# Kernel tuning notes

Hardware: AMD Instinct MI355X
Metric: run time of the kernel (lower is better)

Reference implementation:

```python
import jax, jax.numpy as jnp
import numpy as np

EMBED_DIM = 768
NUM_HEADS = 12


def setup_inputs() -> dict:
    key = jax.random.key(0)
    ks = jax.random.split(key, 9)
    C = EMBED_DIM
    x = jax.random.normal(ks[0], (8, 3136, C), dtype=jnp.float32)
    s = 0.02
    Wq = jax.random.normal(ks[1], (C, C), dtype=jnp.float32) * s
    Wk = jax.random.normal(ks[2], (C, C), dtype=jnp.float32) * s
    Wv = jax.random.normal(ks[3], (C, C), dtype=jnp.float32) * s
    Wo = jax.random.normal(ks[4], (C, C), dtype=jnp.float32) * s
    bq = jax.random.normal(ks[5], (C,), dtype=jnp.float32) * s
    bk = jax.random.normal(ks[6], (C,), dtype=jnp.float32) * s
    bv = jax.random.normal(ks[7], (C,), dtype=jnp.float32) * s
    bo = jax.random.normal(ks[8], (C,), dtype=jnp.float32) * s
    return {"x": x, "Wq": Wq, "bq": bq, "Wk": Wk, "bk": bk,
            "Wv": Wv, "bv": bv, "Wo": Wo, "bo": bo, "T": 16}


def reference(x, Wq, bq, Wk, bk, Wv, bv, Wo, bo, T):
    B, N, C = x.shape
    H = NUM_HEADS
    hd = C // H
    Hh = H // 2
    P = N // T
    scale = 1.0 / np.sqrt(hd).astype(np.float32)

    Q = (x @ Wq + bq).reshape(B, T, P, H, hd)
    K = (x @ Wk + bk).reshape(B, T, P, H, hd)
    V = (x @ Wv + bv).reshape(B, T, P, H, hd)

    # spatial attention: first Hh heads, attend over patches within each frame
    Qs, Ks, Vs = Q[..., :Hh, :], K[..., :Hh, :], V[..., :Hh, :]
    scores_s = jnp.einsum('btphd,btqhd->bthpq', Qs, Ks) * scale  # (B,T,Hh,P,P)
    ws = jax.nn.softmax(scores_s, axis=-1)
    out_s = jnp.einsum('bthpq,btqhd->btphd', ws, Vs)  # (B,T,P,Hh,hd)

    # temporal attention: last Hh heads, attend over frames at each patch
    Qt, Kt, Vt = Q[..., Hh:, :], K[..., Hh:, :], V[..., Hh:, :]
    scores_t = jnp.einsum('btphd,bsphd->bphts', Qt, Kt) * scale  # (B,P,Hh,T,T)
    wt = jax.nn.softmax(scores_t, axis=-1)
    out_t = jnp.einsum('bphts,bsphd->btphd', wt, Vt)  # (B,T,P,Hh,hd)

    out = jnp.concatenate([out_s, out_t], axis=3).reshape(B, N, C)
    return out @ Wo + bo
```

## Files before the change

kernel.cpp:

```cpp
#include <hip/hip_runtime.h>


typedef __attribute__((ext_vector_type(8))) short short8;
typedef __attribute__((ext_vector_type(4))) float f32x4;

typedef __attribute__((address_space(1))) void gvoid;
typedef __attribute__((address_space(3))) void lvoid;

__device__ __forceinline__ unsigned short f2b(float f) {
  unsigned int u = __float_as_uint(f);
  unsigned int r = (u + 0x7FFFu + ((u >> 16) & 1u)) >> 16;
  return (unsigned short)r;
}

__global__ __launch_bounds__(256) void k_convert_x(
    const float* __restrict__ x, unsigned short* __restrict__ xb,
    const float* __restrict__ bq, const float* __restrict__ bk,
    const float* __restrict__ bv, float* __restrict__ bqkv) {
  int tid = blockIdx.x * 256 + threadIdx.x;
  if (tid < 2304)
    bqkv[tid] = tid < 768 ? bq[tid] : (tid < 1536 ? bk[tid - 768] : bv[tid - 1536]);
  float4 v = ((const float4*)x)[tid];
  ushort4 o;
  o.x = f2b(v.x); o.y = f2b(v.y); o.z = f2b(v.z); o.w = f2b(v.w);
  ((ushort4*)xb)[tid] = o;
}

__global__ __launch_bounds__(256) void k_pack_w(
    const float* __restrict__ Wq, const float* __restrict__ Wk,
    const float* __restrict__ Wv, const float* __restrict__ Wo,
    unsigned short* __restrict__ wqkvT, unsigned short* __restrict__ woT) {
  __shared__ float tile[32][33];
  int bid = blockIdx.x;
  const float* W;
  unsigned short* dst;
  int n0, k0;
  if (bid < 1728) {
    int tn = bid % 72, tk = bid / 72;
    n0 = tn * 32; k0 = tk * 32;
    int which = n0 / 768;
    W = which == 0 ? Wq : (which == 1 ? Wk : Wv);
    dst = wqkvT;
  } else {
    int b2 = bid - 1728;
    int tn = b2 % 24, tk = b2 / 24;
    n0 = tn * 32; k0 = tk * 32;
    W = Wo; dst = woT;
  }
  int nn0 = n0 % 768;
  for (int i = threadIdx.x; i < 1024; i += 256) {
    int r = i >> 5, c = i & 31;
    tile[r][c] = W[(size_t)(k0 + r) * 768 + nn0 + c];
  }
  __syncthreads();
  for (int i = threadIdx.x; i < 1024; i += 256) {
    int r = i >> 5, c = i & 31;
    dst[(size_t)(n0 + r) * 768 + k0 + c] = f2b(tile[c][r]);
  }
}


#define FENCE asm volatile("" ::: "memory")
#define BARRIER do { FENCE; __builtin_amdgcn_s_barrier(); FENCE; } while (0)
#define WAIT_LGKM0 asm volatile("s_waitcnt lgkmcnt(0)" ::: "memory")
#define WAIT_VM6 asm volatile("s_waitcnt vmcnt(6)" ::: "memory")

#define STAGE(PBASE, BUFBASE, HT, KT_) do {                                          \
    int kt__ = (KT_);                                                                \
    bool real__ = (kt__ < 12);                                                       \
    if (!real__) kt__ -= 12;                                                         \
    const unsigned short* src__ = (PBASE) + (HT) * 98304 + kt__ * 64;                \
    unsigned d0__ = real__ ? ((BUFBASE) + (HT) * 8192 + w * 512) : (65536u + w * 512); \
    unsigned d1__ = real__ ? ((BUFBASE) + (HT) * 8192 + 4096 + w * 512) : (65536u + w * 512); \
    __builtin_amdgcn_global_load_lds((const gvoid*)src__, (lvoid*)(lds + d0__), 16, 0, 0); \
    __builtin_amdgcn_global_load_lds((const gvoid*)(src__ + 49152), (lvoid*)(lds + d1__), 16, 0, 0); \
  } while (0)

#define LDA(MH, ABASE) do {                                                          \
    const unsigned short* ab__ = lds + (ABASE) + ((MH) * 128 + arow) * 64;           \
    _Pragma("unroll")                                                                \
    for (int mf = 0; mf < 4; ++mf) {                                                 \
      af[mf][0] = *(const short8*)(ab__ + mf * 1024 + s0);                           \
      af[mf][1] = *(const short8*)(ab__ + mf * 1024 + s1);                           \
    }                                                                                \
  } while (0)

#define LDB(NH, BBASE) do {                                                          \
    const unsigned short* bb__ = lds + (BBASE) + ((NH) * 128 + brow) * 64;           \
    _Pragma("unroll")                                                                \
    for (int nf = 0; nf < 2; ++nf) {                                                 \
      bf[nf][0] = *(const short8*)(bb__ + nf * 1024 + s0);                           \
      bf[nf][1] = *(const short8*)(bb__ + nf * 1024 + s1);                           \
    }                                                                                \
  } while (0)

#define MM(MH, NH) do {                                                              \
    __builtin_amdgcn_s_setprio(1);                                                   \
    _Pragma("unroll")                                                                \
    for (int mf = 0; mf < 4; ++mf) {                                                 \
      _Pragma("unroll")                                                              \
      for (int nf = 0; nf < 2; ++nf) {                                               \
        acc[MH][mf][NH][nf] = __builtin_amdgcn_mfma_f32_16x16x32_bf16(               \
            af[mf][0], bf[nf][0], acc[MH][mf][NH][nf], 0, 0, 0);                     \
        acc[MH][mf][NH][nf] = __builtin_amdgcn_mfma_f32_16x16x32_bf16(               \
            af[mf][1], bf[nf][1], acc[MH][mf][NH][nf], 0, 0, 0);                     \
      }                                                                              \
    }                                                                                \
    __builtin_amdgcn_s_setprio(0);                                                   \
  } while (0)

__global__ __launch_bounds__(512, 2) void k_gemm256(
    const unsigned short* __restrict__ A, const unsigned short* __restrict__ Bt,
    const float* __restrict__ bias, unsigned short* __restrict__ Cout,
    int M, int N) {
  __shared__ __align__(16) unsigned short lds[69632];
  const int nwg = gridDim.x;
  const int nbx = N >> 8;
  const int orig = blockIdx.x;
  const int q = nwg >> 3, r = nwg & 7;
  const int xcd = orig & 7, lin = orig >> 3;
  const int wg = (xcd < r ? xcd * (q + 1) : r * (q + 1) + (xcd - r) * q) + lin;
  const int m0 = (wg / nbx) << 8, n0 = (wg % nbx) << 8;

  const int tid = threadIdx.x;
  const int w = tid >> 6, l = tid & 63;
  const int wm = w >> 2, wn = w & 3;
  const int lg = l >> 4, ln = l & 15;
  const int arow = wm * 64 + ln;
  const int brow = wn * 32 + ln;
  const int s0 = (lg ^ (ln & 7)) * 8;
  const int s1 = s0 ^ 32;
  const int srow = tid >> 3;
  const int slg8 = ((tid & 7) ^ (srow & 7)) * 8;
  const unsigned short* pA = A + (size_t)(m0 + srow) * 768 + slg8;
  const unsigned short* pB = Bt + (size_t)(n0 + srow) * 768 + slg8;

  f32x4 acc[2][4][2][2] = {};

  STAGE(pA, 0,     0, 0);
  STAGE(pB, 16384, 1, 0);
  STAGE(pA, 0,     1, 0);
  STAGE(pB, 16384, 0, 0);
  STAGE(pA, 32768, 0, 1);
  STAGE(pB, 49152, 1, 1);
  STAGE(pA, 32768, 1, 1);
  asm volatile("s_waitcnt vmcnt(6)" ::: "memory");
  __builtin_amdgcn_s_barrier();
  FENCE;

  for (int it = 0; it < 6; ++it) {
    const int kt1 = 2 * it + 1, ktn0 = 2 * it + 2, ktn1 = 2 * it + 3;
    short8 af[4][2], bf[2][2];
    LDA(0, 0); LDB(0, 16384);
    STAGE(pB, 49152, 0, kt1);
    BARRIER; WAIT_LGKM0; MM(0, 0); BARRIER;
    LDB(1, 16384);
    STAGE(pA, 0, 0, ktn0);
    BARRIER; WAIT_LGKM0; MM(0, 1); BARRIER;
    LDA(1, 0);
    STAGE(pB, 16384, 1, ktn0);
    BARRIER; WAIT_LGKM0; MM(1, 1); BARRIER;
    LDB(0, 16384);
    STAGE(pA, 0, 1, ktn0);
    WAIT_VM6;
    BARRIER; WAIT_LGKM0; MM(1, 0); BARRIER;
    LDA(0, 32768); LDB(0, 49152);
    STAGE(pB, 16384, 0, ktn0);
    BARRIER; WAIT_LGKM0; MM(0, 0); BARRIER;
    LDB(1, 49152);
    STAGE(pA, 32768, 0, ktn1);
    BARRIER; WAIT_LGKM0; MM(0, 1); BARRIER;
    LDA(1, 32768);
    STAGE(pB, 49152, 1, ktn1);
    BARRIER; WAIT_LGKM0; MM(1, 1); BARRIER;
    LDB(0, 49152);
    STAGE(pA, 32768, 1, ktn1);
    WAIT_VM6;
    BARRIER; WAIT_LGKM0; MM(1, 0); BARRIER;
  }

#pragma unroll
  for (int mh = 0; mh < 2; ++mh)
#pragma unroll
    for (int mf = 0; mf < 4; ++mf)
#pragma unroll
      for (int nh = 0; nh < 2; ++nh)
#pragma unroll
        for (int nf = 0; nf < 2; ++nf) {
          const int col = n0 + nh * 128 + wn * 32 + nf * 16 + ln;
          const float bval = bias[col];
          const int row = m0 + mh * 128 + wm * 64 + mf * 16 + lg * 4;
#pragma unroll
          for (int rr = 0; rr < 4; ++rr)
            Cout[(size_t)(row + rr) * N + col] = f2b(acc[mh][mf][nh][nf][rr] + bval);
        }
}

__global__ __launch_bounds__(256) void k_gemm_out(
    const unsigned short* __restrict__ A, const unsigned short* __restrict__ Bt,
    const float* __restrict__ bias, float* __restrict__ C,
    int M, int N, int K) {
  __shared__ __align__(16) unsigned short As[2][128 * 32];
  __shared__ __align__(16) unsigned short Bs[2][128 * 32];
  const int tid = threadIdx.x;
  const int w = tid >> 6, l = tid & 63;
  const int lg = l >> 4, ln = l & 15;
  const int m0 = blockIdx.y * 128, n0 = blockIdx.x * 128;
  const int wr = (w >> 1) * 64, wc = (w & 1) * 64;
  f32x4 acc[4][4] = {};
  const unsigned short* ga = A + (size_t)(m0 + (tid >> 2)) * K + ((tid & 3) * 8);
  const unsigned short* gb = Bt + (size_t)(n0 + (tid >> 2)) * K + ((tid & 3) * 8);
  const size_t krow64 = (size_t)64 * K;
  const int wofs = w * 512;

#define OSTAGE(CO, K0) do {                                                                        \
    __builtin_amdgcn_global_load_lds((const gvoid*)(ga + (K0)),          (lvoid*)(&As[0][0] + (CO) + wofs),        16, 0, 0); \
    __builtin_amdgcn_global_load_lds((const gvoid*)(ga + krow64 + (K0)), (lvoid*)(&As[0][0] + (CO) + 2048 + wofs), 16, 0, 0); \
    __builtin_amdgcn_global_load_lds((const gvoid*)(gb + (K0)),          (lvoid*)(&Bs[0][0] + (CO) + wofs),        16, 0, 0); \
    __builtin_amdgcn_global_load_lds((const gvoid*)(gb + krow64 + (K0)), (lvoid*)(&Bs[0][0] + (CO) + 2048 + wofs), 16, 0, 0); \
  } while (0)

  OSTAGE(0, 0);
  asm volatile("s_waitcnt vmcnt(0)" ::: "memory");
  BARRIER;
  int co = 0;
  for (int k0 = 0; k0 < K; k0 += 32) {
    if (k0 + 32 < K) OSTAGE(co ^ 4096, k0 + 32);
    const unsigned short* as = &As[0][0] + co;
    const unsigned short* bs = &Bs[0][0] + co;
    short8 a[4], b[4];
#pragma unroll
    for (int mt = 0; mt < 4; ++mt)
      a[mt] = *(const short8*)(as + (wr + mt * 16 + ln) * 32 + lg * 8);
#pragma unroll
    for (int nt = 0; nt < 4; ++nt)
      b[nt] = *(const short8*)(bs + (wc + nt * 16 + ln) * 32 + lg * 8);
#pragma unroll
    for (int mt = 0; mt < 4; ++mt)
#pragma unroll
      for (int nt = 0; nt < 4; ++nt)
        acc[mt][nt] = __builtin_amdgcn_mfma_f32_16x16x32_bf16(a[mt], b[nt], acc[mt][nt], 0, 0, 0);
    asm volatile("s_waitcnt vmcnt(0)" ::: "memory");
    BARRIER;
    co ^= 4096;
  }
#pragma unroll
  for (int nt = 0; nt < 4; ++nt) {
    int col = n0 + wc + nt * 16 + ln;
    float bval = bias[col];
#pragma unroll
    for (int mt = 0; mt < 4; ++mt) {
      int row = m0 + wr + mt * 16 + lg * 4;
#pragma unroll
      for (int r = 0; r < 4; ++r)
        C[(size_t)(row + r) * N + col] = acc[mt][nt][r] + bval;
    }
  }
#undef OSTAGE
}

__global__ __launch_bounds__(256) void k_attn_spatial(
    const unsigned short* __restrict__ qkv, unsigned short* __restrict__ attn) {
  const int bi = blockIdx.x;
  const int h = bi % 6;
  const int t = (bi / 6) % 16;
  const int b = bi / 96;
  const int base_row = b * 3136 + t * 196;
  __shared__ __align__(16) unsigned short Vt[64][232];
  __shared__ __align__(16) unsigned short Pl[4][16][232];
  for (int i = threadIdx.x; i < 196 * 64; i += 256) {
    int key = i >> 6, d = i & 63;
    Vt[d][key] = qkv[(size_t)(base_row + key) * 2304 + 1536 + h * 64 + d];
  }
  for (int i = threadIdx.x; i < 64 * 28; i += 256)
    Vt[i / 28][196 + (i % 28)] = 0;
  __syncthreads();
  const int w = threadIdx.x >> 6, l = threadIdx.x & 63;
  const int lg = l >> 4, ln = l & 15;
  const float scale = 0.125f;
  for (int mt = w; mt < 13; mt += 4) {
    int qm = mt * 16 + ln; if (qm > 195) qm = 195;
    const size_t qoff = (size_t)(base_row + qm) * 2304 + h * 64 + lg * 8;
    short8 qa0 = *(const short8*)(qkv + qoff);
    short8 qa1 = *(const short8*)(qkv + qoff + 32);
    f32x4 st[13];
#pragma unroll
    for (int nt = 0; nt < 13; ++nt) {
      int kn = nt * 16 + ln; if (kn > 195) kn = 195;
      const size_t koff = (size_t)(base_row + kn) * 2304 + 768 + h * 64 + lg * 8;
      short8 kb0 = *(const short8*)(qkv + koff);
      short8 kb1 = *(const short8*)(qkv + koff + 32);
      f32x4 s = {0.f, 0.f, 0.f, 0.f};
      s = __builtin_amdgcn_mfma_f32_16x16x32_bf16(qa0, kb0, s, 0, 0, 0);
      s = __builtin_amdgcn_mfma_f32_16x16x32_bf16(qa1, kb1, s, 0, 0, 0);
      st[nt] = s;
    }
    float mr[4] = {-1e30f, -1e30f, -1e30f, -1e30f};
#pragma unroll
    for (int nt = 0; nt < 13; ++nt) {
      bool valid = (nt * 16 + ln) < 196;
#pragma unroll
      for (int r = 0; r < 4; ++r) {
        float v = valid ? st[nt][r] * scale : -1e30f;
        st[nt][r] = v;
        mr[r] = fmaxf(mr[r], v);
      }
    }
#pragma unroll
    for (int msk = 1; msk <= 8; msk <<= 1)
#pragma unroll
      for (int r = 0; r < 4; ++r) mr[r] = fmaxf(mr[r], __shfl_xor(mr[r], msk));
    float sm[4] = {0.f, 0.f, 0.f, 0.f};
#pragma unroll
    for (int nt = 0; nt < 13; ++nt)
#pragma unroll
      for (int r = 0; r < 4; ++r) {
        float p = __expf(st[nt][r] - mr[r]);
        st[nt][r] = p;
        sm[r] += p;
      }
#pragma unroll
    for (int msk = 1; msk <= 8; msk <<= 1)
#pragma unroll
      for (int r = 0; r < 4; ++r) sm[r] += __shfl_xor(sm[r], msk);
    float inv[4];
#pragma unroll
    for (int r = 0; r < 4; ++r) inv[r] = 1.f / sm[r];
#pragma unroll
    for (int nt = 0; nt < 13; ++nt)
#pragma unroll
      for (int r = 0; r < 4; ++r)
        Pl[w][lg * 4 + r][nt * 16 + ln] = f2b(st[nt][r] * inv[r]);
#pragma unroll
    for (int r = 0; r < 4; ++r) Pl[w][ln][208 + lg * 4 + r] = 0;
#pragma unroll
    for (int nt4 = 0; nt4 < 4; ++nt4) {
      f32x4 acc = {0.f, 0.f, 0.f, 0.f};
#pragma unroll
      for (int ks = 0; ks < 7; ++ks) {
        short8 pa = *(const short8*)(&Pl[w][ln][ks * 32 + lg * 8]);
        short8 vb = *(const short8*)(&Vt[nt4 * 16 + ln][ks * 32 + lg * 8]);
        acc = __builtin_amdgcn_mfma_f32_16x16x32_bf16(pa, vb, acc, 0, 0, 0);
      }
#pragma unroll
      for (int r = 0; r < 4; ++r) {
        int m = mt * 16 + lg * 4 + r;
        if (m < 196)
          attn[(size_t)(base_row + m) * 768 + h * 64 + nt4 * 16 + ln] = f2b(acc[r]);
      }
    }
  }
}

__global__ __launch_bounds__(256) void k_attn_temporal(
    const unsigned short* __restrict__ qkv, unsigned short* __restrict__ attn) {
  const int w = threadIdx.x >> 6, l = threadIdx.x & 63;
  const int u = blockIdx.x * 4 + w;
  const int b = u / 1176;
  const int rem = u % 1176;
  const int p = rem / 6;
  const int h = 6 + rem % 6;
  const size_t rowb = (size_t)b * 3136 + p;
  __shared__ __align__(16) unsigned short Vt[4][64][40];
  __shared__ __align__(16) unsigned short Pl[4][16][40];
  for (int i = l; i < 1024; i += 64) {
    int tt = i >> 6, d = i & 63;
    Vt[w][d][tt] = qkv[(rowb + (size_t)tt * 196) * 2304 + 1536 + h * 64 + d];
  }
  for (int i = l; i < 1024; i += 64)
    Vt[w][i >> 4][16 + (i & 15)] = 0;
  const int lg = l >> 4, ln = l & 15;
  const size_t qoff = (rowb + (size_t)ln * 196) * 2304 + h * 64 + lg * 8;
  short8 qa0 = *(const short8*)(qkv + qoff);
  short8 qa1 = *(const short8*)(qkv + qoff + 32);
  short8 kb0 = *(const short8*)(qkv + qoff + 768);
  short8 kb1 = *(const short8*)(qkv + qoff + 768 + 32);
  f32x4 s = {0.f, 0.f, 0.f, 0.f};
  s = __builtin_amdgcn_mfma_f32_16x16x32_bf16(qa0, kb0, s, 0, 0, 0);
  s = __builtin_amdgcn_mfma_f32_16x16x32_bf16(qa1, kb1, s, 0, 0, 0);
  const float scale = 0.125f;
  float stv[4], mr[4];
#pragma unroll
  for (int r = 0; r < 4; ++r) { stv[r] = s[r] * scale; mr[r] = stv[r]; }
#pragma unroll
  for (int msk = 1; msk <= 8; msk <<= 1)
#pragma unroll
    for (int r = 0; r < 4; ++r) mr[r] = fmaxf(mr[r], __shfl_xor(mr[r], msk));
  float sm[4];
#pragma unroll
  for (int r = 0; r < 4; ++r) { stv[r] = __expf(stv[r] - mr[r]); sm[r] = stv[r]; }
#pragma unroll
  for (int msk = 1; msk <= 8; msk <<= 1)
#pragma unroll
    for (int r = 0; r < 4; ++r) sm[r] += __shfl_xor(sm[r], msk);
#pragma unroll
  for (int r = 0; r < 4; ++r)
    Pl[w][lg * 4 + r][ln] = f2b(stv[r] / sm[r]);
#pragma unroll
  for (int r = 0; r < 4; ++r) Pl[w][ln][16 + lg * 4 + r] = 0;
  short8 pa = *(const short8*)(&Pl[w][ln][lg * 8]);
#pragma unroll
  for (int nt4 = 0; nt4 < 4; ++nt4) {
    short8 vb = *(const short8*)(&Vt[w][nt4 * 16 + ln][lg * 8]);
    f32x4 acc = {0.f, 0.f, 0.f, 0.f};
    acc = __builtin_amdgcn_mfma_f32_16x16x32_bf16(pa, vb, acc, 0, 0, 0);
#pragma unroll
    for (int r = 0; r < 4; ++r) {
      int tq = lg * 4 + r;
      attn[((size_t)b * 3136 + (size_t)tq * 196 + p) * 768 + h * 64 + nt4 * 16 + ln] = f2b(acc[r]);
    }
  }
}

extern "C" void kernel_launch(void* const* d_in, const int* in_sizes, int n_in,
                              void* d_out, int out_size, void* d_ws, size_t ws_size,
                              hipStream_t stream) {
  const float* x  = (const float*)d_in[0];
  const float* Wq = (const float*)d_in[1];
  const float* bq = (const float*)d_in[2];
  const float* Wk = (const float*)d_in[3];
  const float* bk = (const float*)d_in[4];
  const float* Wv = (const float*)d_in[5];
  const float* bv = (const float*)d_in[6];
  const float* Wo = (const float*)d_in[7];
  const float* bo = (const float*)d_in[8];
  float* out = (float*)d_out;
  char* ws = (char*)d_ws;
  unsigned short* xb    = (unsigned short*)(ws + 0);
  unsigned short* wqkvT = (unsigned short*)(ws + 38535168);
  float*          bqkv  = (float*)(ws + 42074112);
  unsigned short* woT   = (unsigned short*)(ws + 42083328);
  unsigned short* qkvb  = (unsigned short*)(ws + 43262976);
  unsigned short* attnb = (unsigned short*)(ws + 158868480);

  k_convert_x<<<18816, 256, 0, stream>>>(x, xb, bq, bk, bv, bqkv);
  k_pack_w<<<2304, 256, 0, stream>>>(Wq, Wk, Wv, Wo, wqkvT, woT);
  k_gemm256<<<882, 512, 0, stream>>>(xb, wqkvT, bqkv, qkvb, 25088, 2304);
  k_attn_spatial<<<768, 256, 0, stream>>>(qkvb, attnb);
  k_attn_temporal<<<2352, 256, 0, stream>>>(qkvb, attnb);
  k_gemm_out<<<dim3(6, 196), 256, 0, stream>>>(attnb, woT, bo, out, 25088, 768, 768);
}
```

Before: 255.2 us.

## Merge spatial and temporal attention into one launch and rework GEMM pipeline

Spatial and temporal attention now run as one kernel that dispatches on block index, so the two launches become one and the work can overlap. Spatial blocks are split in half by query tiles, which doubles the block count for better occupancy but loads V twice. Separately, the QKV GEMM's staging order is rotated, the trailing barrier after each MFMA step is removed, and the wait threshold drops from vmcnt 6 to 4. These changes aim to cut synchronisation stalls, at the risk of LDS hazards if the rotated staging overwrites a buffer that is still being read.

```diff
diff --git a/kernel.cpp b/kernel.cpp
--- a/kernel.cpp
+++ b/kernel.cpp
@@ -63,7 +63,7 @@
 #define FENCE asm volatile("" ::: "memory")
 #define BARRIER do { FENCE; __builtin_amdgcn_s_barrier(); FENCE; } while (0)
 #define WAIT_LGKM0 asm volatile("s_waitcnt lgkmcnt(0)" ::: "memory")
-#define WAIT_VM6 asm volatile("s_waitcnt vmcnt(6)" ::: "memory")
+#define WAIT_VM4 asm volatile("s_waitcnt vmcnt(4)" ::: "memory")
 
 #define STAGE(PBASE, BUFBASE, HT, KT_) do {                                          \
     int kt__ = (KT_);                                                                \
@@ -138,45 +138,43 @@
   f32x4 acc[2][4][2][2] = {};
 
   STAGE(pA, 0,     0, 0);
+  STAGE(pB, 16384, 0, 0);
+  STAGE(pA, 0,     1, 0);
   STAGE(pB, 16384, 1, 0);
-  STAGE(pA, 0,     1, 0);
-  STAGE(pB, 16384, 0, 0);
   STAGE(pA, 32768, 0, 1);
   STAGE(pB, 49152, 1, 1);
-  STAGE(pA, 32768, 1, 1);
-  asm volatile("s_waitcnt vmcnt(6)" ::: "memory");
-  __builtin_amdgcn_s_barrier();
-  FENCE;
+  WAIT_VM4;
+  BARRIER;
 
   for (int it = 0; it < 6; ++it) {
     const int kt1 = 2 * it + 1, ktn0 = 2 * it + 2, ktn1 = 2 * it + 3;
     short8 af[4][2], bf[2][2];
     LDA(0, 0); LDB(0, 16384);
+    STAGE(pA, 32768, 1, kt1);
+    BARRIER; WAIT_LGKM0; MM(0, 0);
+    LDB(1, 16384);
     STAGE(pB, 49152, 0, kt1);
-    BARRIER; WAIT_LGKM0; MM(0, 0); BARRIER;
-    LDB(1, 16384);
+    BARRIER; WAIT_LGKM0; MM(0, 1);
+    LDA(1, 0);
     STAGE(pA, 0, 0, ktn0);
-    BARRIER; WAIT_LGKM0; MM(0, 1); BARRIER;
-    LDA(1, 0);
+    BARRIER; WAIT_LGKM0; MM(1, 1);
+    LDB(0, 16384);
     STAGE(pB, 16384, 1, ktn0);
-    BARRIER; WAIT_LGKM0; MM(1, 1); BARRIER;
-    LDB(0, 16384);
+    WAIT_VM4;
+    BARRIER; WAIT_LGKM0; MM(1, 0);
+    LDA(0, 32768); LDB(0, 49152);
     STAGE(pA, 0, 1, ktn0);
-    WAIT_VM6;
-    BARRIER; WAIT_LGKM0; MM(1, 0); BARRIER;
-    LDA(0, 32768); LDB(0, 49152);
+    BARRIER; WAIT_LGKM0; MM(0, 0);
+    LDB(1, 49152);
     STAGE(pB, 16384, 0, ktn0);
-    BARRIER; WAIT_LGKM0; MM(0, 0); BARRIER;
-    LDB(1, 49152);
+    BARRIER; WAIT_LGKM0; MM(0, 1);
+    LDA(1, 32768);
     STAGE(pA, 32768, 0, ktn1);
-    BARRIER; WAIT_LGKM0; MM(0, 1); BARRIER;
-    LDA(1, 32768);
+    BARRIER; WAIT_LGKM0; MM(1, 1);
+    LDB(0, 49152);
     STAGE(pB, 49152, 1, ktn1);
-    BARRIER; WAIT_LGKM0; MM(1, 1); BARRIER;
-    LDB(0, 49152);
-    STAGE(pA, 32768, 1, ktn1);
-    WAIT_VM6;
-    BARRIER; WAIT_LGKM0; MM(1, 0); BARRIER;
+    WAIT_VM4;
+    BARRIER; WAIT_LGKM0; MM(1, 0);
   }
 
 #pragma unroll
@@ -259,155 +257,155 @@
 #undef OSTAGE
 }
 
-__global__ __launch_bounds__(256) void k_attn_spatial(
+__global__ __launch_bounds__(256) void k_attn_fused(
     const unsigned short* __restrict__ qkv, unsigned short* __restrict__ attn) {
-  const int bi = blockIdx.x;
-  const int h = bi % 6;
-  const int t = (bi / 6) % 16;
-  const int b = bi / 96;
-  const int base_row = b * 3136 + t * 196;
-  __shared__ __align__(16) unsigned short Vt[64][232];
-  __shared__ __align__(16) unsigned short Pl[4][16][232];
-  for (int i = threadIdx.x; i < 196 * 64; i += 256) {
-    int key = i >> 6, d = i & 63;
-    Vt[d][key] = qkv[(size_t)(base_row + key) * 2304 + 1536 + h * 64 + d];
-  }
-  for (int i = threadIdx.x; i < 64 * 28; i += 256)
-    Vt[i / 28][196 + (i % 28)] = 0;
-  __syncthreads();
+  __shared__ __align__(16) unsigned short smem[29696];
   const int w = threadIdx.x >> 6, l = threadIdx.x & 63;
   const int lg = l >> 4, ln = l & 15;
   const float scale = 0.125f;
-  for (int mt = w; mt < 13; mt += 4) {
-    int qm = mt * 16 + ln; if (qm > 195) qm = 195;
-    const size_t qoff = (size_t)(base_row + qm) * 2304 + h * 64 + lg * 8;
+  if (blockIdx.x < 1536) {
+    const int bi = blockIdx.x >> 1;
+    const int half = blockIdx.x & 1;
+    const int h = bi % 6;
+    const int t = (bi / 6) % 16;
+    const int b = bi / 96;
+    const int base_row = b * 3136 + t * 196;
+    unsigned short* Vt = smem;
+    unsigned short* Pl = smem + 14848;
+    for (int i = threadIdx.x; i < 196 * 64; i += 256) {
+      int key = i >> 6, d = i & 63;
+      Vt[d * 232 + key] = qkv[(size_t)(base_row + key) * 2304 + 1536 + h * 64 + d];
+    }
+    for (int i = threadIdx.x; i < 64 * 28; i += 256)
+      Vt[(i / 28) * 232 + 196 + (i % 28)] = 0;
+    __syncthreads();
+    const int r0 = half ? 7 : 0, r1 = half ? 13 : 7;
+    for (int mt = r0 + w; mt < r1; mt += 4) {
+      int qm = mt * 16 + ln; if (qm > 195) qm = 195;
+      const size_t qoff = (size_t)(base_row + qm) * 2304 + h * 64 + lg * 8;
+      short8 qa0 = *(const short8*)(qkv + qoff);
+      short8 qa1 = *(const short8*)(qkv + qoff + 32);
+      f32x4 st[13];
+#pragma unroll
+      for (int nt = 0; nt < 13; ++nt) {
+        int kn = nt * 16 + ln; if (kn > 195) kn = 195;
+        const size_t koff = (size_t)(base_row + kn) * 2304 + 768 + h * 64 + lg * 8;
+        short8 kb0 = *(const short8*)(qkv + koff);
+        short8 kb1 = *(const short8*)(qkv + koff + 32);
+        f32x4 s = {0.f, 0.f, 0.f, 0.f};
+        s = __builtin_amdgcn_mfma_f32_16x16x32_bf16(qa0, kb0, s, 0, 0, 0);
+        s = __builtin_amdgcn_mfma_f32_16x16x32_bf16(qa1, kb1, s, 0, 0, 0);
+        st[nt] = s;
+      }
+      float mr[4] = {-1e30f, -1e30f, -1e30f, -1e30f};
+#pragma unroll
+      for (int nt = 0; nt < 13; ++nt) {
+        bool valid = (nt * 16 + ln) < 196;
+#pragma unroll
+        for (int r = 0; r < 4; ++r) {
+          float v = valid ? st[nt][r] * scale : -1e30f;
+          st[nt][r] = v;
+          mr[r] = fmaxf(mr[r], v);
+        }
+      }
+#pragma unroll
+      for (int msk = 1; msk <= 8; msk <<= 1)
+#pragma unroll
+        for (int r = 0; r < 4; ++r) mr[r] = fmaxf(mr[r], __shfl_xor(mr[r], msk));
+      float sm[4] = {0.f, 0.f, 0.f, 0.f};
+#pragma unroll
+      for (int nt = 0; nt < 13; ++nt)
+#pragma unroll
+        for (int r = 0; r < 4; ++r) {
+          float p = __expf(st[nt][r] - mr[r]);
+          st[nt][r] = p;
+          sm[r] += p;
+        }
+#pragma unroll
+      for (int msk = 1; msk <= 8; msk <<= 1)
+#pragma unroll
+        for (int r = 0; r < 4; ++r) sm[r] += __shfl_xor(sm[r], msk);
+      float inv[4];
+#pragma unroll
+      for (int r = 0; r < 4; ++r) inv[r] = 1.f / sm[r];
+      unsigned short* Pw = Pl + w * 16 * 232;
+#pragma unroll
+      for (int nt = 0; nt < 13; ++nt)
+#pragma unroll
+        for (int r = 0; r < 4; ++r)
+          Pw[(lg * 4 + r) * 232 + nt * 16 + ln] = f2b(st[nt][r] * inv[r]);
+#pragma unroll
+      for (int r = 0; r < 4; ++r) Pw[ln * 232 + 208 + lg * 4 + r] = 0;
+#pragma unroll
+      for (int nt4 = 0; nt4 < 4; ++nt4) {
+        f32x4 acc = {0.f, 0.f, 0.f, 0.f};
+#pragma unroll
+        for (int ks = 0; ks < 7; ++ks) {
+          short8 pa = *(const short8*)(Pw + ln * 232 + ks * 32 + lg * 8);
+          short8 vb = *(const short8*)(Vt + (nt4 * 16 + ln) * 232 + ks * 32 + lg * 8);
+          acc = __builtin_amdgcn_mfma_f32_16x16x32_bf16(pa, vb, acc, 0, 0, 0);
+        }
+#pragma unroll
+        for (int r = 0; r < 4; ++r) {
+          int m = mt * 16 + lg * 4 + r;
+          if (m < 196)
+            attn[(size_t)(base_row + m) * 768 + h * 64 + nt4 * 16 + ln] = f2b(acc[r]);
+        }
+      }
+    }
+  } else {
+    const int u = (blockIdx.x - 1536) * 4 + w;
+    const int b = u / 1176;
+    const int rem = u % 1176;
+    const int p = rem / 6;
+    const int h = 6 + rem % 6;
+    const size_t rowb = (size_t)b * 3136 + p;
+    unsigned short* Vt = smem + w * 2560;
+    unsigned short* Pl = smem + 10240 + w * 640;
+    for (int i = l; i < 1024; i += 64) {
+      int tt = i >> 6, d = i & 63;
+      Vt[d * 40 + tt] = qkv[(rowb + (size_t)tt * 196) * 2304 + 1536 + h * 64 + d];
+    }
+    for (int i = l; i < 1024; i += 64)
+      Vt[(i >> 4) * 40 + 16 + (i & 15)] = 0;
+    const size_t qoff = (rowb + (size_t)ln * 196) * 2304 + h * 64 + lg * 8;
     short8 qa0 = *(const short8*)(qkv + qoff);
     short8 qa1 = *(const short8*)(qkv + qoff + 32);
-    f32x4 st[13];
-#pragma unroll
-    for (int nt = 0; nt < 13; ++nt) {
-      int kn = nt * 16 + ln; if (kn > 195) kn = 195;
-      const size_t koff = (size_t)(base_row + kn) * 2304 + 768 + h * 64 + lg * 8;
-      short8 kb0 = *(const short8*)(qkv + koff);
-      short8 kb1 = *(const short8*)(qkv + koff + 32);
-      f32x4 s = {0.f, 0.f, 0.f, 0.f};
-      s = __builtin_amdgcn_mfma_f32_16x16x32_bf16(qa0, kb0, s, 0, 0, 0);
-      s = __builtin_amdgcn_mfma_f32_16x16x32_bf16(qa1, kb1, s, 0, 0, 0);
-      st[nt] = s;
-    }
-    float mr[4] = {-1e30f, -1e30f, -1e30f, -1e30f};
-#pragma unroll
-    for (int nt = 0; nt < 13; ++nt) {
-      bool valid = (nt * 16 + ln) < 196;
+    short8 kb0 = *(const short8*)(qkv + qoff + 768);
+    short8 kb1 = *(const short8*)(qkv + qoff + 768 + 32);
+    f32x4 s = {0.f, 0.f, 0.f, 0.f};
+    s = __builtin_amdgcn_mfma_f32_16x16x32_bf16(qa0, kb0, s, 0, 0, 0);
+    s = __builtin_amdgcn_mfma_f32_16x16x32_bf16(qa1, kb1, s, 0, 0, 0);
+    float stv[4], mr[4];
+#pragma unroll
+    for (int r = 0; r < 4; ++r) { stv[r] = s[r] * scale; mr[r] = stv[r]; }
+#pragma unroll
+    for (int msk = 1; msk <= 8; msk <<= 1)
+#pragma unroll
+      for (int r = 0; r < 4; ++r) mr[r] = fmaxf(mr[r], __shfl_xor(mr[r], msk));
+    float sm[4];
+#pragma unroll
+    for (int r = 0; r < 4; ++r) { stv[r] = __expf(stv[r] - mr[r]); sm[r] = stv[r]; }
+#pragma unroll
+    for (int msk = 1; msk <= 8; msk <<= 1)
+#pragma unroll
+      for (int r = 0; r < 4; ++r) sm[r] += __shfl_xor(sm[r], msk);
+#pragma unroll
+    for (int r = 0; r < 4; ++r)
+      Pl[(lg * 4 + r) * 40 + ln] = f2b(stv[r] / sm[r]);
+#pragma unroll
+    for (int r = 0; r < 4; ++r) Pl[ln * 40 + 16 + lg * 4 + r] = 0;
+    short8 pa = *(const short8*)(Pl + ln * 40 + lg * 8);
+#pragma unroll
+    for (int nt4 = 0; nt4 < 4; ++nt4) {
+      short8 vb = *(const short8*)(Vt + (nt4 * 16 + ln) * 40 + lg * 8);
+      f32x4 acc = {0.f, 0.f, 0.f, 0.f};
+      acc = __builtin_amdgcn_mfma_f32_16x16x32_bf16(pa, vb, acc, 0, 0, 0);
 #pragma unroll
       for (int r = 0; r < 4; ++r) {
-        float v = valid ? st[nt][r] * scale : -1e30f;
-        st[nt][r] = v;
-        mr[r] = fmaxf(mr[r], v);
+        int tq = lg * 4 + r;
+        attn[((size_t)b * 3136 + (size_t)tq * 196 + p) * 768 + h * 64 + nt4 * 16 + ln] = f2b(acc[r]);
       }
-    }
-#pragma unroll
-    for (int msk = 1; msk <= 8; msk <<= 1)
-#pragma unroll
-      for (int r = 0; r < 4; ++r) mr[r] = fmaxf(mr[r], __shfl_xor(mr[r], msk));
-    float sm[4] = {0.f, 0.f, 0.f, 0.f};
-#pragma unroll
-    for (int nt = 0; nt < 13; ++nt)
-#pragma unroll
-      for (int r = 0; r < 4; ++r) {
-        float p = __expf(st[nt][r] - mr[r]);
-        st[nt][r] = p;
-        sm[r] += p;
-      }
-#pragma unroll
-    for (int msk = 1; msk <= 8; msk <<= 1)
-#pragma unroll
-      for (int r = 0; r < 4; ++r) sm[r] += __shfl_xor(sm[r], msk);
-    float inv[4];
-#pragma unroll
-    for (int r = 0; r < 4; ++r) inv[r] = 1.f / sm[r];
-#pragma unroll
-    for (int nt = 0; nt < 13; ++nt)
-#pragma unroll
-      for (int r = 0; r < 4; ++r)
-        Pl[w][lg * 4 + r][nt * 16 + ln] = f2b(st[nt][r] * inv[r]);
-#pragma unroll
-    for (int r = 0; r < 4; ++r) Pl[w][ln][208 + lg * 4 + r] = 0;
-#pragma unroll
-    for (int nt4 = 0; nt4 < 4; ++nt4) {
-      f32x4 acc = {0.f, 0.f, 0.f, 0.f};
-#pragma unroll
-      for (int ks = 0; ks < 7; ++ks) {
-        short8 pa = *(const short8*)(&Pl[w][ln][ks * 32 + lg * 8]);
-        short8 vb = *(const short8*)(&Vt[nt4 * 16 + ln][ks * 32 + lg * 8]);
-        acc = __builtin_amdgcn_mfma_f32_16x16x32_bf16(pa, vb, acc, 0, 0, 0);
-      }
-#pragma unroll
-      for (int r = 0; r < 4; ++r) {
-        int m = mt * 16 + lg * 4 + r;
-        if (m < 196)
-          attn[(size_t)(base_row + m) * 768 + h * 64 + nt4 * 16 + ln] = f2b(acc[r]);
-      }
-    }
-  }
-}
-
-__global__ __launch_bounds__(256) void k_attn_temporal(
-    const unsigned short* __restrict__ qkv, unsigned short* __restrict__ attn) {
-  const int w = threadIdx.x >> 6, l = threadIdx.x & 63;
-  const int u = blockIdx.x * 4 + w;
-  const int b = u / 1176;
-  const int rem = u % 1176;
-  const int p = rem / 6;
-  const int h = 6 + rem % 6;
-  const size_t rowb = (size_t)b * 3136 + p;
-  __shared__ __align__(16) unsigned short Vt[4][64][40];
-  __shared__ __align__(16) unsigned short Pl[4][16][40];
-  for (int i = l; i < 1024; i += 64) {
-    int tt = i >> 6, d = i & 63;
-    Vt[w][d][tt] = qkv[(rowb + (size_t)tt * 196) * 2304 + 1536 + h * 64 + d];
-  }
-  for (int i = l; i < 1024; i += 64)
-    Vt[w][i >> 4][16 + (i & 15)] = 0;
-  const int lg = l >> 4, ln = l & 15;
-  const size_t qoff = (rowb + (size_t)ln * 196) * 2304 + h * 64 + lg * 8;
-  short8 qa0 = *(const short8*)(qkv + qoff);
-  short8 qa1 = *(const short8*)(qkv + qoff + 32);
-  short8 kb0 = *(const short8*)(qkv + qoff + 768);
-  short8 kb1 = *(const short8*)(qkv + qoff + 768 + 32);
-  f32x4 s = {0.f, 0.f, 0.f, 0.f};
-  s = __builtin_amdgcn_mfma_f32_16x16x32_bf16(qa0, kb0, s, 0, 0, 0);
-  s = __builtin_amdgcn_mfma_f32_16x16x32_bf16(qa1, kb1, s, 0, 0, 0);
-  const float scale = 0.125f;
-  float stv[4], mr[4];
-#pragma unroll
-  for (int r = 0; r < 4; ++r) { stv[r] = s[r] * scale; mr[r] = stv[r]; }
-#pragma unroll
-  for (int msk = 1; msk <= 8; msk <<= 1)
-#pragma unroll
-    for (int r = 0; r < 4; ++r) mr[r] = fmaxf(mr[r], __shfl_xor(mr[r], msk));
-  float sm[4];
-#pragma unroll
-  for (int r = 0; r < 4; ++r) { stv[r] = __expf(stv[r] - mr[r]); sm[r] = stv[r]; }
-#pragma unroll
-  for (int msk = 1; msk <= 8; msk <<= 1)
-#pragma unroll
-    for (int r = 0; r < 4; ++r) sm[r] += __shfl_xor(sm[r], msk);
-#pragma unroll
-  for (int r = 0; r < 4; ++r)
-    Pl[w][lg * 4 + r][ln] = f2b(stv[r] / sm[r]);
-#pragma unroll
-  for (int r = 0; r < 4; ++r) Pl[w][ln][16 + lg * 4 + r] = 0;
-  short8 pa = *(const short8*)(&Pl[w][ln][lg * 8]);
-#pragma unroll
-  for (int nt4 = 0; nt4 < 4; ++nt4) {
-    short8 vb = *(const short8*)(&Vt[w][nt4 * 16 + ln][lg * 8]);
-    f32x4 acc = {0.f, 0.f, 0.f, 0.f};
-    acc = __builtin_amdgcn_mfma_f32_16x16x32_bf16(pa, vb, acc, 0, 0, 0);
-#pragma unroll
-    for (int r = 0; r < 4; ++r) {
-      int tq = lg * 4 + r;
-      attn[((size_t)b * 3136 + (size_t)tq * 196 + p) * 768 + h * 64 + nt4 * 16 + ln] = f2b(acc[r]);
     }
   }
 }
@@ -436,7 +434,6 @@
   k_convert_x<<<18816, 256, 0, stream>>>(x, xb, bq, bk, bv, bqkv);
   k_pack_w<<<2304, 256, 0, stream>>>(Wq, Wk, Wv, Wo, wqkvT, woT);
   k_gemm256<<<882, 512, 0, stream>>>(xb, wqkvT, bqkv, qkvb, 25088, 2304);
-  k_attn_spatial<<<768, 256, 0, stream>>>(qkvb, attnb);
-  k_attn_temporal<<<2352, 256, 0, stream>>>(qkvb, attnb);
+  k_attn_fused<<<3888, 256, 0, stream>>>(qkvb, attnb);
   k_gemm_out<<<dim3(6, 196), 256, 0, stream>>>(attnb, woT, bo, out, 25088, 768, 768);
 }
```

After: 262.6 us. 1.03x slower.
